# Kernel optimization log

Hardware: AMD Instinct MI355X
Metric: run time of the kernel (lower is better)

## Reference

```python
import jax, jax.numpy as jnp
import numpy as np

STRIDE = 8  # window over x[:, max(0, i-stride) : i+1]


def setup_inputs() -> dict:
    key = jax.random.key(0)
    k0, k1, k2, k3, k4 = jax.random.split(key, 5)
    B, T, H = 16, 8192, 256
    x = jax.random.normal(k0, (B, T, H), dtype=jnp.float32)
    s = 1.0 / np.sqrt(H)  # torch nn.Linear default init range
    W_lin = jax.random.uniform(k1, (H, H), jnp.float32, -s, s)
    b_lin = jax.random.uniform(k2, (H,), jnp.float32, -s, s)
    W_mem = jax.random.uniform(k3, (H, H), jnp.float32, -s, s)
    b_mem = jax.random.uniform(k4, (H,), jnp.float32, -s, s)
    return {"x": x, "W_lin": W_lin, "b_lin": b_lin, "W_mem": W_mem, "b_mem": b_mem}


def reference(x, W_lin, b_lin, W_mem, b_mem):
    # x: [B, T, H]; input_dim == hidden_dim so input_lin is None in the original.
    B, T, H = x.shape
    # h = Linear(x)  (torch Linear: x @ W.T + b)
    h = jnp.einsum('bth,oh->bto', x, W_lin) + b_lin
    # Causal sliding-window mean over window [max(0, t-STRIDE), t] via cumsum.
    cs = jnp.cumsum(x, axis=1)                       # [B, T, H]
    idx = jnp.arange(T)
    start = jnp.maximum(0, idx - STRIDE)             # [T]
    prev = jnp.where((start > 0)[None, :, None],
                     cs[:, jnp.maximum(start - 1, 0)], 0.0)
    counts = (idx - start + 1).astype(x.dtype)       # min(t+1, STRIDE+1)
    means = (cs - prev) / counts[None, :, None]      # [B, T, H]
    # memory branch: Linear over window means, batched as one matmul
    mem = jnp.einsum('bth,oh->bto', means, W_mem) + b_mem
    return h + mem
```

## Files before the change

### kernel.cpp

```cpp
#include <hip/hip_runtime.h>
#include <hip/hip_bf16.h>

#define B_ 16
#define T_ 8192
#define H_ 256
#define M_ (B_ * T_)
#define K_ 512
#define STRIDE_ 8

typedef __bf16 bf16x8 __attribute__((ext_vector_type(8)));
typedef float f32x4 __attribute__((ext_vector_type(4)));

__device__ __forceinline__ unsigned short f2bf(float f) {
  unsigned u = __builtin_bit_cast(unsigned, f);
  u += 0x7fffu + ((u >> 16) & 1u);
  return (unsigned short)(u >> 16);
}

__device__ __forceinline__ void load_lds16(const void* g, void* l) {
  __builtin_amdgcn_global_load_lds(
      (const __attribute__((address_space(1))) void*)g,
      (__attribute__((address_space(3))) void*)l, 16, 0, 0);
}

__global__ __launch_bounds__(256) void wcat_kernel(
    const float* __restrict__ Wl, const float* __restrict__ bl,
    const float* __restrict__ Wm, const float* __restrict__ bm,
    unsigned short* __restrict__ Wcat, float* __restrict__ bias) {
  const int e = blockIdx.x * 256 + threadIdx.x;
  const int o = e >> 9;
  const int k = e & 511;
  const float w = (k < 256) ? Wl[o * 256 + k] : Wm[o * 256 + (k - 256)];
  Wcat[e] = f2bf(w);
  if (e < 256) bias[e] = bl[e] + bm[e];
}

__global__ __launch_bounds__(256, 4) void fused_kernel(
    const float* __restrict__ x,
    const unsigned short* __restrict__ Wc,
    const float* __restrict__ bias,
    float* __restrict__ out) {
  __shared__ __align__(16) unsigned short As[128 * 32];
  __shared__ __align__(16) unsigned short Bs[128 * 32];
  const int tid = threadIdx.x;
  const int m0 = blockIdx.x << 7;
  const int n0 = blockIdx.y << 7;
  const int tb0 = m0 & (T_ - 1);
  const int w = tid >> 6;
  const int l = tid & 63;
  const int wr = (w >> 1) << 6;
  const int wc = (w & 1) << 6;
  const int lm = l & 15;
  const int kq = (l >> 4) << 3;

  const int f0 = tid, f1 = tid + 256;
  const size_t gb0 = (size_t)(n0 + (f0 >> 2)) * 512 + ((f0 & 3) << 3);
  const size_t gb1 = (size_t)(n0 + (f1 >> 2)) * 512 + ((f1 & 3) << 3);

  const int p_cp = tid & 15, p_g = tid >> 4;
  const int q_c = tid & 31, q_g = tid >> 5;

  f32x4 acc[4][4];
#pragma unroll
  for (int i = 0; i < 4; ++i)
#pragma unroll
    for (int j = 0; j < 4; ++j) acc[i][j] = (f32x4){0.f, 0.f, 0.f, 0.f};

  for (int kc = 0; kc < 16; ++kc) {
    __syncthreads();
    load_lds16(Wc + gb0 + kc * 32, &Bs[f0 * 8]);
    load_lds16(Wc + gb1 + kc * 32, &Bs[f1 * 8]);

    if (kc < 8) {
      const int c = kc * 32;
      const float2* __restrict__ x2 =
          (const float2*)x + (size_t)(m0 + p_g * 8) * 128 + (c >> 1) + p_cp;
      unsigned* __restrict__ As32 = (unsigned*)As;
#pragma unroll
      for (int r = 0; r < 8; ++r) {
        const float2 v = x2[(size_t)r * 128];
        As32[(p_g * 8 + r) * 16 + p_cp] =
            (unsigned)f2bf(v.x) | ((unsigned)f2bf(v.y) << 16);
      }
    } else {
      const int c = kc * 32 - 256;
      float v[24];
#pragma unroll
      for (int i = 0; i < 24; ++i) {
        const int lr = q_g * 16 - 8 + i;
        const bool ok = (tb0 + lr) >= 0;
        v[i] = ok ? x[(size_t)(m0 + lr) * 256 + c + q_c] : 0.f;
      }
      float s = 0.f;
#pragma unroll
      for (int i = 0; i < 8; ++i) s += v[i];
#pragma unroll
      for (int r = 0; r < 16; ++r) {
        s += v[r + 8];
        const int t = tb0 + q_g * 16 + r;
        const float inv =
            (t >= STRIDE_) ? (1.f / 9.f) : __builtin_amdgcn_rcpf((float)(t + 1));
        As[(q_g * 16 + r) * 32 + q_c] = f2bf(s * inv);
        s -= v[r];
      }
    }
    __syncthreads();

    bf16x8 a[4], bb[4];
#pragma unroll
    for (int i = 0; i < 4; ++i)
      a[i] = *(const bf16x8*)&As[(wr + i * 16 + lm) * 32 + kq];
#pragma unroll
    for (int j = 0; j < 4; ++j)
      bb[j] = *(const bf16x8*)&Bs[(wc + j * 16 + lm) * 32 + kq];
#pragma unroll
    for (int i = 0; i < 4; ++i)
#pragma unroll
      for (int j = 0; j < 4; ++j)
        acc[i][j] =
            __builtin_amdgcn_mfma_f32_16x16x32_bf16(a[i], bb[j], acc[i][j], 0, 0, 0);
  }

  const int r0 = (l >> 4) << 2;
#pragma unroll
  for (int j = 0; j < 4; ++j) {
    const int o = n0 + wc + j * 16 + lm;
    const float bs = bias[o];
#pragma unroll
    for (int i = 0; i < 4; ++i) {
      const size_t mr = (size_t)(m0 + wr + i * 16 + r0);
#pragma unroll
      for (int r = 0; r < 4; ++r) out[(mr + r) * 256 + o] = acc[i][j][r] + bs;
    }
  }
}

extern "C" void kernel_launch(void* const* d_in, const int* in_sizes, int n_in,
                              void* d_out, int out_size, void* d_ws, size_t ws_size,
                              hipStream_t stream) {
  const float* x  = (const float*)d_in[0];
  const float* Wl = (const float*)d_in[1];
  const float* bl = (const float*)d_in[2];
  const float* Wm = (const float*)d_in[3];
  const float* bm = (const float*)d_in[4];
  float* out = (float*)d_out;

  char* ws = (char*)d_ws;
  unsigned short* Wcat = (unsigned short*)ws;
  float* bias = (float*)(ws + (size_t)256 * 512 * 2);

  wcat_kernel<<<512, 256, 0, stream>>>(Wl, bl, Wm, bm, Wcat, bias);
  fused_kernel<<<dim3(M_ / 128, 2), 256, 0, stream>>>(x, Wcat, bias, out);
}
```

Measured before the change: 332.6 us.

## Retile GEMM to 64x256 blocks with swizzled pre-packed weights and fused x/mean staging

Each block now computes 64 rows across all 256 output columns, so x is read once per row block instead of twice across two column tiles. Both the x slice and its window mean for the same channel slice are staged together per iteration. Weights are pre-packed per iteration in an XOR-swizzled layout, so plain 16-byte global-to-LDS copies land already swizzled and avoid LDS bank conflicts on the fragment reads. The cost is larger LDS use (40 KB per block) and occupancy lowered to 3 blocks per SIMD, and every block reloads the full 32 KB weight slice each iteration.

Result: faster. 270.4 us (-18.7%).

```diff
diff --git a/kernel.cpp b/kernel.cpp
--- a/kernel.cpp
+++ b/kernel.cpp
@@ -5,7 +5,6 @@
 #define T_ 8192
 #define H_ 256
 #define M_ (B_ * T_)
-#define K_ 512
 #define STRIDE_ 8
 
 typedef __bf16 bf16x8 __attribute__((ext_vector_type(8)));
@@ -26,39 +25,39 @@
 __global__ __launch_bounds__(256) void wcat_kernel(
     const float* __restrict__ Wl, const float* __restrict__ bl,
     const float* __restrict__ Wm, const float* __restrict__ bm,
-    unsigned short* __restrict__ Wcat, float* __restrict__ bias) {
+    unsigned short* __restrict__ Wpk, float* __restrict__ bias) {
   const int e = blockIdx.x * 256 + threadIdx.x;
-  const int o = e >> 9;
-  const int k = e & 511;
-  const float w = (k < 256) ? Wl[o * 256 + k] : Wm[o * 256 + (k - 256)];
-  Wcat[e] = f2bf(w);
+  const int it = e >> 14;
+  const int r = (e >> 6) & 255;
+  const int col = e & 63;
+  const int cp = col >> 3;
+  const int ei = col & 7;
+  const int c = cp ^ (r & 7);
+  const int k = it * 32 + (c & 3) * 8 + ei + ((c < 4) ? 0 : 256);
+  const float w = (k < 256) ? Wl[r * 256 + k] : Wm[r * 256 + (k - 256)];
+  Wpk[e] = f2bf(w);
   if (e < 256) bias[e] = bl[e] + bm[e];
 }
 
-__global__ __launch_bounds__(256, 4) void fused_kernel(
+__global__ __launch_bounds__(256, 3) void fused_kernel(
     const float* __restrict__ x,
-    const unsigned short* __restrict__ Wc,
+    const unsigned short* __restrict__ Wpk,
     const float* __restrict__ bias,
     float* __restrict__ out) {
-  __shared__ __align__(16) unsigned short As[128 * 32];
-  __shared__ __align__(16) unsigned short Bs[128 * 32];
+  __shared__ __align__(16) unsigned short As[64 * 64];
+  __shared__ __align__(16) unsigned short Bs[256 * 64];
   const int tid = threadIdx.x;
-  const int m0 = blockIdx.x << 7;
-  const int n0 = blockIdx.y << 7;
+  const int m0 = blockIdx.x << 6;
   const int tb0 = m0 & (T_ - 1);
   const int w = tid >> 6;
   const int l = tid & 63;
-  const int wr = (w >> 1) << 6;
-  const int wc = (w & 1) << 6;
+  const int wc = w << 6;
   const int lm = l & 15;
-  const int kq = (l >> 4) << 3;
+  const int kqc = l >> 4;
 
-  const int f0 = tid, f1 = tid + 256;
-  const size_t gb0 = (size_t)(n0 + (f0 >> 2)) * 512 + ((f0 & 3) << 3);
-  const size_t gb1 = (size_t)(n0 + (f1 >> 2)) * 512 + ((f1 & 3) << 3);
-
-  const int p_cp = tid & 15, p_g = tid >> 4;
-  const int q_c = tid & 31, q_g = tid >> 5;
+  const int p = tid & 15, g = tid >> 4;
+  const float2* __restrict__ x2 = (const float2*)x;
+  unsigned* __restrict__ As32 = (unsigned*)As;
 
   f32x4 acc[4][4];
 #pragma unroll
@@ -66,69 +65,77 @@
 #pragma unroll
     for (int j = 0; j < 4; ++j) acc[i][j] = (f32x4){0.f, 0.f, 0.f, 0.f};
 
-  for (int kc = 0; kc < 16; ++kc) {
+  for (int it = 0; it < 8; ++it) {
     __syncthreads();
-    load_lds16(Wc + gb0 + kc * 32, &Bs[f0 * 8]);
-    load_lds16(Wc + gb1 + kc * 32, &Bs[f1 * 8]);
 
-    if (kc < 8) {
-      const int c = kc * 32;
-      const float2* __restrict__ x2 =
-          (const float2*)x + (size_t)(m0 + p_g * 8) * 128 + (c >> 1) + p_cp;
-      unsigned* __restrict__ As32 = (unsigned*)As;
+    const unsigned short* bsrc = Wpk + (it << 14);
 #pragma unroll
-      for (int r = 0; r < 8; ++r) {
-        const float2 v = x2[(size_t)r * 128];
-        As32[(p_g * 8 + r) * 16 + p_cp] =
-            (unsigned)f2bf(v.x) | ((unsigned)f2bf(v.y) << 16);
-      }
-    } else {
-      const int c = kc * 32 - 256;
-      float v[24];
+    for (int rnd = 0; rnd < 8; ++rnd) {
+      const int f = tid + (rnd << 8);
+      load_lds16(bsrc + f * 8, &Bs[f * 8]);
+    }
+
+    float2 v[12];
 #pragma unroll
-      for (int i = 0; i < 24; ++i) {
-        const int lr = q_g * 16 - 8 + i;
-        const bool ok = (tb0 + lr) >= 0;
-        v[i] = ok ? x[(size_t)(m0 + lr) * 256 + c + q_c] : 0.f;
-      }
-      float s = 0.f;
+    for (int i = 0; i < 12; ++i) {
+      const int rl = (g << 2) - 8 + i;
+      float2 val = {0.f, 0.f};
+      if (tb0 + rl >= 0)
+        val = x2[(size_t)(m0 + rl) * 128 + (it << 4) + p];
+      v[i] = val;
+    }
+    float sx = 0.f, sy = 0.f;
 #pragma unroll
-      for (int i = 0; i < 8; ++i) s += v[i];
+    for (int i = 0; i < 8; ++i) { sx += v[i].x; sy += v[i].y; }
 #pragma unroll
-      for (int r = 0; r < 16; ++r) {
-        s += v[r + 8];
-        const int t = tb0 + q_g * 16 + r;
-        const float inv =
-            (t >= STRIDE_) ? (1.f / 9.f) : __builtin_amdgcn_rcpf((float)(t + 1));
-        As[(q_g * 16 + r) * 32 + q_c] = f2bf(s * inv);
-        s -= v[r];
-      }
+    for (int rr = 0; rr < 4; ++rr) {
+      sx += v[rr + 8].x; sy += v[rr + 8].y;
+      const int r = (g << 2) + rr;
+      const int t = tb0 + r;
+      const float inv =
+          (t >= STRIDE_) ? (1.f / 9.f) : __builtin_amdgcn_rcpf((float)(t + 1));
+      const unsigned xp =
+          (unsigned)f2bf(v[rr + 8].x) | ((unsigned)f2bf(v[rr + 8].y) << 16);
+      const unsigned mp =
+          (unsigned)f2bf(sx * inv) | ((unsigned)f2bf(sy * inv) << 16);
+      const int sw = r & 7;
+      As32[r * 32 + (((p >> 2) ^ sw) << 2) + (p & 3)] = xp;
+      As32[r * 32 + (((4 + (p >> 2)) ^ sw) << 2) + (p & 3)] = mp;
+      sx -= v[rr].x; sy -= v[rr].y;
     }
     __syncthreads();
 
-    bf16x8 a[4], bb[4];
 #pragma unroll
-    for (int i = 0; i < 4; ++i)
-      a[i] = *(const bf16x8*)&As[(wr + i * 16 + lm) * 32 + kq];
+    for (int kk = 0; kk < 2; ++kk) {
+      const int cc = (kk << 2) + kqc;
+      bf16x8 a[4], bb[4];
 #pragma unroll
-    for (int j = 0; j < 4; ++j)
-      bb[j] = *(const bf16x8*)&Bs[(wc + j * 16 + lm) * 32 + kq];
+      for (int i = 0; i < 4; ++i) {
+        const int R = (i << 4) + lm;
+        a[i] = *(const bf16x8*)&As[R * 64 + ((cc ^ (R & 7)) << 3)];
+      }
 #pragma unroll
-    for (int i = 0; i < 4; ++i)
+      for (int j = 0; j < 4; ++j) {
+        const int R = wc + (j << 4) + lm;
+        bb[j] = *(const bf16x8*)&Bs[R * 64 + ((cc ^ (R & 7)) << 3)];
+      }
 #pragma unroll
-      for (int j = 0; j < 4; ++j)
-        acc[i][j] =
-            __builtin_amdgcn_mfma_f32_16x16x32_bf16(a[i], bb[j], acc[i][j], 0, 0, 0);
+      for (int i = 0; i < 4; ++i)
+#pragma unroll
+        for (int j = 0; j < 4; ++j)
+          acc[i][j] = __builtin_amdgcn_mfma_f32_16x16x32_bf16(a[i], bb[j],
+                                                              acc[i][j], 0, 0, 0);
+    }
   }
 
   const int r0 = (l >> 4) << 2;
 #pragma unroll
   for (int j = 0; j < 4; ++j) {
-    const int o = n0 + wc + j * 16 + lm;
+    const int o = wc + (j << 4) + lm;
     const float bs = bias[o];
 #pragma unroll
     for (int i = 0; i < 4; ++i) {
-      const size_t mr = (size_t)(m0 + wr + i * 16 + r0);
+      const size_t mr = (size_t)(m0 + (i << 4) + r0);
 #pragma unroll
       for (int r = 0; r < 4; ++r) out[(mr + r) * 256 + o] = acc[i][j][r] + bs;
     }
@@ -146,9 +153,9 @@
   float* out = (float*)d_out;
 
   char* ws = (char*)d_ws;
-  unsigned short* Wcat = (unsigned short*)ws;
-  float* bias = (float*)(ws + (size_t)256 * 512 * 2);
+  unsigned short* Wpk = (unsigned short*)ws;
+  float* bias = (float*)(ws + (size_t)8 * 256 * 64 * 2);
 
-  wcat_kernel<<<512, 256, 0, stream>>>(Wl, bl, Wm, bm, Wcat, bias);
-  fused_kernel<<<dim3(M_ / 128, 2), 256, 0, stream>>>(x, Wcat, bias, out);
+  wcat_kernel<<<512, 256, 0, stream>>>(Wl, bl, Wm, bm, Wpk, bias);
+  fused_kernel<<<2048, 256, 0, stream>>>(x, Wpk, bias, out);
 }
```
